# Performance work log

Hardware: AMD Instinct MI355X
Metric: run time of the kernel (lower is better)

## Reference

```python
import jax, jax.numpy as jnp
import numpy as np

N_NODES = 1_000_000
N_GRAPHS = 4096
EPS = 1e-16


def setup_inputs() -> dict:
    key = jax.random.key(0)
    ks = jax.random.split(key, 9)
    x = jax.random.normal(ks[0], (N_NODES, 64), dtype=jnp.float32)
    node_batch = jnp.sort(jax.random.randint(ks[1], (N_NODES,), 0, N_GRAPHS)).astype(jnp.int64)
    global_attr = jax.random.normal(ks[2], (N_GRAPHS, 3), dtype=jnp.float32)
    s3, s128, s64 = 1.0 / np.sqrt(3.0), 1.0 / np.sqrt(128.0), 1.0 / np.sqrt(64.0)
    Wg = jax.random.uniform(ks[3], (3, 64), minval=-s3, maxval=s3, dtype=jnp.float32)
    bg = jax.random.uniform(ks[4], (64,), minval=-s3, maxval=s3, dtype=jnp.float32)
    Wn = jax.random.uniform(ks[5], (128, 64), minval=-s128, maxval=s128, dtype=jnp.float32)
    bn = jax.random.uniform(ks[6], (64,), minval=-s128, maxval=s128, dtype=jnp.float32)
    Wa = jax.random.uniform(ks[7], (64, 1), minval=-s64, maxval=s64, dtype=jnp.float32)
    ba = jax.random.uniform(ks[8], (1,), minval=-s64, maxval=s64, dtype=jnp.float32)
    return {"x": x, "node_batch": node_batch, "global_attr": global_attr,
            "Wg": Wg, "bg": bg, "Wn": Wn, "bn": bn, "Wa": Wa, "ba": ba}


def _segment_softmax(scores, seg, num_segments):
    # scores: [N]; seg: [N] int ids. Numerically stable per-segment softmax.
    m = jax.ops.segment_max(scores, seg, num_segments=num_segments)
    e = jnp.exp(scores - m[seg])
    denom = jax.ops.segment_sum(e, seg, num_segments=num_segments)
    return e / (denom[seg] + EPS)


def reference(x, node_batch, global_attr, Wg, bg, Wn, bn, Wa, ba):
    seg = node_batch.astype(jnp.int32)
    g = global_attr @ Wg + bg                    # [B, 64]
    graph_embed = g[seg]                         # repeat_interleave broadcast -> [N, 64]
    chunk = jnp.concatenate([x, graph_embed], axis=-1)   # [N, 128]
    h = jax.nn.softplus(chunk @ Wn + bn)         # [N, 64]
    s = (h @ Wa + ba)[:, 0]                      # [N]
    w = _segment_softmax(s, seg, N_GRAPHS)       # [N]
    return w[:, None]                            # [N, 1]
```

## Files before the change

kernel.cpp:

```cpp
#include <hip/hip_runtime.h>
#include <hip/hip_bf16.h>
#include <stdint.h>

#define N_NODES_C 1000000
#define N_GRAPHS_C 4096

typedef __attribute__((ext_vector_type(8))) __bf16 bf16x8;
typedef __attribute__((ext_vector_type(4))) float f32x4;

__device__ __forceinline__ unsigned short f2bf(float f) {
    union { float f; unsigned int u; } v; v.f = f;
    unsigned int r = v.u + 0x7FFFu + ((v.u >> 16) & 1u);
    return (unsigned short)(r >> 16);
}
__device__ __forceinline__ unsigned int pack2(float a, float b) {
    return (unsigned int)f2bf(a) | ((unsigned int)f2bf(b) << 16);
}

__global__ __launch_bounds__(256) void stage0_kernel(
    const float* __restrict__ ga, const float* __restrict__ Wg,
    const float* __restrict__ bg, const float* __restrict__ Wn,
    const float* __restrict__ bn,
    float* __restrict__ c, unsigned short* __restrict__ BT,
    float* __restrict__ denom)
{
    __shared__ float Wns[64 * 64];
    __shared__ float gs[4][64];
    int t = threadIdx.x;
#pragma unroll
    for (int i = 0; i < 4; ++i)
        ((float4*)Wns)[t + i * 256] = ((const float4*)(Wn + 64 * 64))[t + i * 256];
    if (blockIdx.x == 0) {
#pragma unroll
        for (int i = 0; i < 16; ++i) {
            int flat = t * 16 + i;
            int n = flat >> 6, k = flat & 63;
            BT[flat] = f2bf(Wn[k * 64 + n]);
        }
    }
    int gl = t >> 6, j = t & 63;
    int b = blockIdx.x * 4 + gl;
    float acc = bg[j];
#pragma unroll
    for (int m = 0; m < 3; ++m) acc += ga[b * 3 + m] * Wg[m * 64 + j];
    gs[gl][j] = acc;
    __syncthreads();
    float cj = bn[j];
#pragma unroll 16
    for (int k = 0; k < 64; ++k) cj += gs[gl][k] * Wns[k * 64 + j];
    c[b * 64 + j] = cj;
    if (j == 0) denom[b] = 0.0f;
}

__global__ __launch_bounds__(256, 4) void node_kernel(
    const float* __restrict__ x, const int* __restrict__ nb,
    const float* __restrict__ c, const unsigned short* __restrict__ BT,
    const float* __restrict__ Wa, const float* __restrict__ ba,
    float* __restrict__ e, float* __restrict__ denom)
{
    int t = threadIdx.x;
    int wave = t >> 6, lane = t & 63;
    int quad = lane >> 4, l15 = lane & 15;
    long base = (long)blockIdx.x * 256 + wave * 64;
    bool is64 = nb[N_NODES_C - 1] < 1024;

    bf16x8 bfrag[4][2];
#pragma unroll
    for (int nt = 0; nt < 4; ++nt)
#pragma unroll
        for (int kh = 0; kh < 2; ++kh)
            bfrag[nt][kh] = *(const bf16x8*)&BT[(nt * 16 + l15) * 64 + quad * 8 + kh * 32];

    float wa[4];
    float bav = ba[0];
#pragma unroll
    for (int nt = 0; nt < 4; ++nt) wa[nt] = Wa[nt * 16 + l15];

#pragma unroll
    for (int t4 = 0; t4 < 4; ++t4) {
        long arow = base + t4 * 16 + l15;
        float4 v0 = make_float4(0.f, 0.f, 0.f, 0.f), v1 = v0, v2 = v0, v3 = v0;
        if (arow < N_NODES_C) {
            const float4* xp = (const float4*)(x + arow * 64);
            v0 = xp[quad * 2];
            v1 = xp[quad * 2 + 1];
            v2 = xp[8 + quad * 2];
            v3 = xp[8 + quad * 2 + 1];
        }
        union { bf16x8 v; unsigned int u[4]; } A0, A1;
        A0.u[0] = pack2(v0.x, v0.y); A0.u[1] = pack2(v0.z, v0.w);
        A0.u[2] = pack2(v1.x, v1.y); A0.u[3] = pack2(v1.z, v1.w);
        A1.u[0] = pack2(v2.x, v2.y); A1.u[1] = pack2(v2.z, v2.w);
        A1.u[2] = pack2(v3.x, v3.y); A1.u[3] = pack2(v3.z, v3.w);

        f32x4 acc[4];
#pragma unroll
        for (int nt = 0; nt < 4; ++nt) {
            acc[nt] = (f32x4){0.f, 0.f, 0.f, 0.f};
            acc[nt] = __builtin_amdgcn_mfma_f32_16x16x32_bf16(A0.v, bfrag[nt][0], acc[nt], 0, 0, 0);
            acc[nt] = __builtin_amdgcn_mfma_f32_16x16x32_bf16(A1.v, bfrag[nt][1], acc[nt], 0, 0, 0);
        }

        long r0 = base + t4 * 16 + quad * 4;
        int sg0 = 0, sg1 = 0, sg2 = 0, sg3 = 0;
        if (is64) {
            if (r0 + 0 < N_NODES_C) sg0 = nb[2 * (r0 + 0)];
            if (r0 + 1 < N_NODES_C) sg1 = nb[2 * (r0 + 1)];
            if (r0 + 2 < N_NODES_C) sg2 = nb[2 * (r0 + 2)];
            if (r0 + 3 < N_NODES_C) sg3 = nb[2 * (r0 + 3)];
        } else {
            if (r0 + 0 < N_NODES_C) sg0 = nb[r0 + 0];
            if (r0 + 1 < N_NODES_C) sg1 = nb[r0 + 1];
            if (r0 + 2 < N_NODES_C) sg2 = nb[r0 + 2];
            if (r0 + 3 < N_NODES_C) sg3 = nb[r0 + 3];
        }
        bool uni = (sg0 == sg3);
        float sp0 = 0.f, sp1 = 0.f, sp2 = 0.f, sp3 = 0.f;
#pragma unroll
        for (int nt = 0; nt < 4; ++nt) {
            int col = nt * 16 + l15;
            float c0, c1, c2, c3;
            if (uni) { c0 = c[sg0 * 64 + col]; c1 = c0; c2 = c0; c3 = c0; }
            else {
                c0 = c[sg0 * 64 + col]; c1 = c[sg1 * 64 + col];
                c2 = c[sg2 * 64 + col]; c3 = c[sg3 * 64 + col];
            }
            float y0 = acc[nt].x + c0, y1 = acc[nt].y + c1;
            float y2 = acc[nt].z + c2, y3 = acc[nt].w + c3;
            sp0 += __logf(1.f + __expf(y0)) * wa[nt];
            sp1 += __logf(1.f + __expf(y1)) * wa[nt];
            sp2 += __logf(1.f + __expf(y2)) * wa[nt];
            sp3 += __logf(1.f + __expf(y3)) * wa[nt];
        }
#pragma unroll
        for (int off = 1; off < 16; off <<= 1) {
            sp0 += __shfl_xor(sp0, off, 64);
            sp1 += __shfl_xor(sp1, off, 64);
            sp2 += __shfl_xor(sp2, off, 64);
            sp3 += __shfl_xor(sp3, off, 64);
        }
        float e0 = __expf(sp0 + bav), e1 = __expf(sp1 + bav);
        float e2 = __expf(sp2 + bav), e3 = __expf(sp3 + bav);
        if (l15 == 0) {
            if (r0 + 3 < N_NODES_C) {
                *(float4*)&e[r0] = make_float4(e0, e1, e2, e3);
                float s = e0; int cur = sg0;
                if (sg1 == cur) s += e1; else { atomicAdd(&denom[cur], s); cur = sg1; s = e1; }
                if (sg2 == cur) s += e2; else { atomicAdd(&denom[cur], s); cur = sg2; s = e2; }
                if (sg3 == cur) s += e3; else { atomicAdd(&denom[cur], s); cur = sg3; s = e3; }
                atomicAdd(&denom[cur], s);
            } else {
                float ev[4] = {e0, e1, e2, e3};
                int sg[4] = {sg0, sg1, sg2, sg3};
                for (int i = 0; i < 4; ++i) {
                    if (r0 + i < N_NODES_C) {
                        e[r0 + i] = ev[i];
                        atomicAdd(&denom[sg[i]], ev[i]);
                    }
                }
            }
        }
    }
}

__global__ __launch_bounds__(256) void fin_kernel(
    const float* __restrict__ e, const int* __restrict__ nb,
    const float* __restrict__ denom, float* __restrict__ out)
{
    long node0 = (long)(blockIdx.x * 256 + threadIdx.x) * 4;
    if (node0 >= N_NODES_C) return;
    bool is64 = nb[N_NODES_C - 1] < 1024;
    float4 ev = *(const float4*)&e[node0];
    int s0, s1, s2, s3;
    if (is64) {
        int4 a = *(const int4*)&nb[2 * node0];
        int4 b = *(const int4*)&nb[2 * node0 + 4];
        s0 = a.x; s1 = a.z; s2 = b.x; s3 = b.z;
    } else {
        int4 a = *(const int4*)&nb[node0];
        s0 = a.x; s1 = a.y; s2 = a.z; s3 = a.w;
    }
    float4 w;
    w.x = ev.x / denom[s0];
    w.y = ev.y / denom[s1];
    w.z = ev.z / denom[s2];
    w.w = ev.w / denom[s3];
    *(float4*)&out[node0] = w;
}

extern "C" void kernel_launch(void* const* d_in, const int* in_sizes, int n_in,
                              void* d_out, int out_size, void* d_ws, size_t ws_size,
                              hipStream_t stream) {
    const float* x  = (const float*)d_in[0];
    const int*   nb = (const int*)d_in[1];
    const float* ga = (const float*)d_in[2];
    const float* Wg = (const float*)d_in[3];
    const float* bg = (const float*)d_in[4];
    const float* Wn = (const float*)d_in[5];
    const float* bn = (const float*)d_in[6];
    const float* Wa = (const float*)d_in[7];
    const float* ba = (const float*)d_in[8];

    char* ws = (char*)d_ws;
    float* e            = (float*)(ws);
    float* c            = (float*)(ws + 4194304);
    unsigned short* BT  = (unsigned short*)(ws + 4194304 + 1048576);
    float* denom        = (float*)(ws + 4194304 + 1048576 + 8192);

    hipLaunchKernelGGL(stage0_kernel, dim3(N_GRAPHS_C / 4), dim3(256), 0, stream,
                       ga, Wg, bg, Wn, bn, c, BT, denom);
    hipLaunchKernelGGL(node_kernel, dim3((N_NODES_C + 255) / 256), dim3(256), 0, stream,
                       x, nb, c, BT, Wa, ba, e, denom);
    hipLaunchKernelGGL(fin_kernel, dim3((N_NODES_C / 4 + 255) / 256), dim3(256), 0, stream,
                       e, nb, denom, (float*)d_out);
}
```

Baseline: 392.6 us.

## Process one 16-row tile per wave and use hardware bf16 pack conversion

The node kernel now gives each wave a single 16-node tile instead of looping over four, which quadruples the grid (N/64 blocks). x and segment-id loads are issued up front, before the B fragments are loaded, so more memory traffic is in flight per wave. Bounds checks are dropped because N divides evenly by 16. The float-to-bf16 packing uses the hardware cvt_pk_bf16_f32 builtin when it exists. The cost is that every wave reloads the B fragments and Wa, with fewer rows to spread that load over.

Result: slower. 416.9 us (+6.2%).

```diff
diff --git a/kernel.cpp b/kernel.cpp
--- a/kernel.cpp
+++ b/kernel.cpp
@@ -6,6 +6,7 @@
 #define N_GRAPHS_C 4096
 
 typedef __attribute__((ext_vector_type(8))) __bf16 bf16x8;
+typedef __attribute__((ext_vector_type(2))) __bf16 bf16x2;
 typedef __attribute__((ext_vector_type(4))) float f32x4;
 
 __device__ __forceinline__ unsigned short f2bf(float f) {
@@ -14,7 +15,13 @@
     return (unsigned short)(r >> 16);
 }
 __device__ __forceinline__ unsigned int pack2(float a, float b) {
+#if __has_builtin(__builtin_amdgcn_cvt_pk_bf16_f32)
+    bf16x2 r = __builtin_amdgcn_cvt_pk_bf16_f32(a, b);
+    union { bf16x2 v; unsigned int u; } cv; cv.v = r;
+    return cv.u;
+#else
     return (unsigned int)f2bf(a) | ((unsigned int)f2bf(b) << 16);
+#endif
 }
 
 __global__ __launch_bounds__(256) void stage0_kernel(
@@ -61,105 +68,85 @@
     int t = threadIdx.x;
     int wave = t >> 6, lane = t & 63;
     int quad = lane >> 4, l15 = lane & 15;
-    long base = (long)blockIdx.x * 256 + wave * 64;
+    int tile = blockIdx.x * 4 + wave;
+    int base = tile * 16;
     bool is64 = nb[N_NODES_C - 1] < 1024;
 
-    bf16x8 bfrag[4][2];
-#pragma unroll
-    for (int nt = 0; nt < 4; ++nt)
-#pragma unroll
-        for (int kh = 0; kh < 2; ++kh)
-            bfrag[nt][kh] = *(const bf16x8*)&BT[(nt * 16 + l15) * 64 + quad * 8 + kh * 32];
-
+    const float4* xp = (const float4*)(x + (long)(base + l15) * 64);
+    float4 v0 = xp[quad * 2];
+    float4 v1 = xp[quad * 2 + 1];
+    float4 v2 = xp[8 + quad * 2];
+    float4 v3 = xp[8 + quad * 2 + 1];
+
+    int r0 = base + quad * 4;
+    int sg0, sg1, sg2, sg3;
+    if (is64) {
+        sg0 = nb[2L * (r0 + 0)]; sg1 = nb[2L * (r0 + 1)];
+        sg2 = nb[2L * (r0 + 2)]; sg3 = nb[2L * (r0 + 3)];
+    } else {
+        sg0 = nb[r0 + 0]; sg1 = nb[r0 + 1];
+        sg2 = nb[r0 + 2]; sg3 = nb[r0 + 3];
+    }
+
+    bf16x8 b0[4], b1[4];
+#pragma unroll
+    for (int nt = 0; nt < 4; ++nt) {
+        b0[nt] = *(const bf16x8*)&BT[(nt * 16 + l15) * 64 + quad * 8];
+        b1[nt] = *(const bf16x8*)&BT[(nt * 16 + l15) * 64 + quad * 8 + 32];
+    }
     float wa[4];
     float bav = ba[0];
 #pragma unroll
     for (int nt = 0; nt < 4; ++nt) wa[nt] = Wa[nt * 16 + l15];
 
-#pragma unroll
-    for (int t4 = 0; t4 < 4; ++t4) {
-        long arow = base + t4 * 16 + l15;
-        float4 v0 = make_float4(0.f, 0.f, 0.f, 0.f), v1 = v0, v2 = v0, v3 = v0;
-        if (arow < N_NODES_C) {
-            const float4* xp = (const float4*)(x + arow * 64);
-            v0 = xp[quad * 2];
-            v1 = xp[quad * 2 + 1];
-            v2 = xp[8 + quad * 2];
-            v3 = xp[8 + quad * 2 + 1];
+    union { bf16x8 v; unsigned int u[4]; } A0, A1;
+    A0.u[0] = pack2(v0.x, v0.y); A0.u[1] = pack2(v0.z, v0.w);
+    A0.u[2] = pack2(v1.x, v1.y); A0.u[3] = pack2(v1.z, v1.w);
+    A1.u[0] = pack2(v2.x, v2.y); A1.u[1] = pack2(v2.z, v2.w);
+    A1.u[2] = pack2(v3.x, v3.y); A1.u[3] = pack2(v3.z, v3.w);
+
+    f32x4 acc[4];
+#pragma unroll
+    for (int nt = 0; nt < 4; ++nt) {
+        acc[nt] = (f32x4){0.f, 0.f, 0.f, 0.f};
+        acc[nt] = __builtin_amdgcn_mfma_f32_16x16x32_bf16(A0.v, b0[nt], acc[nt], 0, 0, 0);
+        acc[nt] = __builtin_amdgcn_mfma_f32_16x16x32_bf16(A1.v, b1[nt], acc[nt], 0, 0, 0);
+    }
+
+    bool uni = (sg0 == sg3);
+    float sp0 = 0.f, sp1 = 0.f, sp2 = 0.f, sp3 = 0.f;
+#pragma unroll
+    for (int nt = 0; nt < 4; ++nt) {
+        int col = nt * 16 + l15;
+        float c0, c1, c2, c3;
+        if (uni) { c0 = c[sg0 * 64 + col]; c1 = c0; c2 = c0; c3 = c0; }
+        else {
+            c0 = c[sg0 * 64 + col]; c1 = c[sg1 * 64 + col];
+            c2 = c[sg2 * 64 + col]; c3 = c[sg3 * 64 + col];
         }
-        union { bf16x8 v; unsigned int u[4]; } A0, A1;
-        A0.u[0] = pack2(v0.x, v0.y); A0.u[1] = pack2(v0.z, v0.w);
-        A0.u[2] = pack2(v1.x, v1.y); A0.u[3] = pack2(v1.z, v1.w);
-        A1.u[0] = pack2(v2.x, v2.y); A1.u[1] = pack2(v2.z, v2.w);
-        A1.u[2] = pack2(v3.x, v3.y); A1.u[3] = pack2(v3.z, v3.w);
-
-        f32x4 acc[4];
-#pragma unroll
-        for (int nt = 0; nt < 4; ++nt) {
-            acc[nt] = (f32x4){0.f, 0.f, 0.f, 0.f};
-            acc[nt] = __builtin_amdgcn_mfma_f32_16x16x32_bf16(A0.v, bfrag[nt][0], acc[nt], 0, 0, 0);
-            acc[nt] = __builtin_amdgcn_mfma_f32_16x16x32_bf16(A1.v, bfrag[nt][1], acc[nt], 0, 0, 0);
-        }
-
-        long r0 = base + t4 * 16 + quad * 4;
-        int sg0 = 0, sg1 = 0, sg2 = 0, sg3 = 0;
-        if (is64) {
-            if (r0 + 0 < N_NODES_C) sg0 = nb[2 * (r0 + 0)];
-            if (r0 + 1 < N_NODES_C) sg1 = nb[2 * (r0 + 1)];
-            if (r0 + 2 < N_NODES_C) sg2 = nb[2 * (r0 + 2)];
-            if (r0 + 3 < N_NODES_C) sg3 = nb[2 * (r0 + 3)];
-        } else {
-            if (r0 + 0 < N_NODES_C) sg0 = nb[r0 + 0];
-            if (r0 + 1 < N_NODES_C) sg1 = nb[r0 + 1];
-            if (r0 + 2 < N_NODES_C) sg2 = nb[r0 + 2];
-            if (r0 + 3 < N_NODES_C) sg3 = nb[r0 + 3];
-        }
-        bool uni = (sg0 == sg3);
-        float sp0 = 0.f, sp1 = 0.f, sp2 = 0.f, sp3 = 0.f;
-#pragma unroll
-        for (int nt = 0; nt < 4; ++nt) {
-            int col = nt * 16 + l15;
-            float c0, c1, c2, c3;
-            if (uni) { c0 = c[sg0 * 64 + col]; c1 = c0; c2 = c0; c3 = c0; }
-            else {
-                c0 = c[sg0 * 64 + col]; c1 = c[sg1 * 64 + col];
-                c2 = c[sg2 * 64 + col]; c3 = c[sg3 * 64 + col];
-            }
-            float y0 = acc[nt].x + c0, y1 = acc[nt].y + c1;
-            float y2 = acc[nt].z + c2, y3 = acc[nt].w + c3;
-            sp0 += __logf(1.f + __expf(y0)) * wa[nt];
-            sp1 += __logf(1.f + __expf(y1)) * wa[nt];
-            sp2 += __logf(1.f + __expf(y2)) * wa[nt];
-            sp3 += __logf(1.f + __expf(y3)) * wa[nt];
-        }
-#pragma unroll
-        for (int off = 1; off < 16; off <<= 1) {
-            sp0 += __shfl_xor(sp0, off, 64);
-            sp1 += __shfl_xor(sp1, off, 64);
-            sp2 += __shfl_xor(sp2, off, 64);
-            sp3 += __shfl_xor(sp3, off, 64);
-        }
-        float e0 = __expf(sp0 + bav), e1 = __expf(sp1 + bav);
-        float e2 = __expf(sp2 + bav), e3 = __expf(sp3 + bav);
-        if (l15 == 0) {
-            if (r0 + 3 < N_NODES_C) {
-                *(float4*)&e[r0] = make_float4(e0, e1, e2, e3);
-                float s = e0; int cur = sg0;
-                if (sg1 == cur) s += e1; else { atomicAdd(&denom[cur], s); cur = sg1; s = e1; }
-                if (sg2 == cur) s += e2; else { atomicAdd(&denom[cur], s); cur = sg2; s = e2; }
-                if (sg3 == cur) s += e3; else { atomicAdd(&denom[cur], s); cur = sg3; s = e3; }
-                atomicAdd(&denom[cur], s);
-            } else {
-                float ev[4] = {e0, e1, e2, e3};
-                int sg[4] = {sg0, sg1, sg2, sg3};
-                for (int i = 0; i < 4; ++i) {
-                    if (r0 + i < N_NODES_C) {
-                        e[r0 + i] = ev[i];
-                        atomicAdd(&denom[sg[i]], ev[i]);
-                    }
-                }
-            }
-        }
+        float y0 = acc[nt].x + c0, y1 = acc[nt].y + c1;
+        float y2 = acc[nt].z + c2, y3 = acc[nt].w + c3;
+        sp0 += __logf(1.f + __expf(y0)) * wa[nt];
+        sp1 += __logf(1.f + __expf(y1)) * wa[nt];
+        sp2 += __logf(1.f + __expf(y2)) * wa[nt];
+        sp3 += __logf(1.f + __expf(y3)) * wa[nt];
+    }
+#pragma unroll
+    for (int off = 1; off < 16; off <<= 1) {
+        sp0 += __shfl_xor(sp0, off, 64);
+        sp1 += __shfl_xor(sp1, off, 64);
+        sp2 += __shfl_xor(sp2, off, 64);
+        sp3 += __shfl_xor(sp3, off, 64);
+    }
+    float e0 = __expf(sp0 + bav), e1 = __expf(sp1 + bav);
+    float e2 = __expf(sp2 + bav), e3 = __expf(sp3 + bav);
+    if (l15 == 0) {
+        *(float4*)&e[r0] = make_float4(e0, e1, e2, e3);
+        float s = e0; int cur = sg0;
+        if (sg1 == cur) s += e1; else { atomicAdd(&denom[cur], s); cur = sg1; s = e1; }
+        if (sg2 == cur) s += e2; else { atomicAdd(&denom[cur], s); cur = sg2; s = e2; }
+        if (sg3 == cur) s += e3; else { atomicAdd(&denom[cur], s); cur = sg3; s = e3; }
+        atomicAdd(&denom[cur], s);
     }
 }
 
@@ -209,7 +196,7 @@
 
     hipLaunchKernelGGL(stage0_kernel, dim3(N_GRAPHS_C / 4), dim3(256), 0, stream,
                        ga, Wg, bg, Wn, bn, c, BT, denom);
-    hipLaunchKernelGGL(node_kernel, dim3((N_NODES_C + 255) / 256), dim3(256), 0, stream,
+    hipLaunchKernelGGL(node_kernel, dim3(N_NODES_C / 64), dim3(256), 0, stream,
                        x, nb, c, BT, Wa, ba, e, denom);
     hipLaunchKernelGGL(fin_kernel, dim3((N_NODES_C / 4 + 255) / 256), dim3(256), 0, stream,
                        e, nb, denom, (float*)d_out);
```
